# Optimization experiments

Measured on AMD Instinct MI355X. Metric: run time of the kernel, lower is better.

## Reference

```python
import jax, jax.numpy as jnp
import numpy as np

N = 50000      # nodes
E = 800000     # edges
IN = 128       # in_dim
OUT = 128      # out_dim
R = 4          # num_relations
H = 8          # heads
D = OUT // H   # per-head dim
NEG_SLOPE = 0.2


def setup_inputs() -> dict:
    key = jax.random.key(0)
    ks = jax.random.split(key, 12)
    s = 0.05
    return {
        "node_inp": jax.random.normal(ks[0], (N, IN), dtype=jnp.float32),
        "edge_index": jax.random.randint(ks[1], (2, E), 0, N),
        "edge_type": jax.random.randint(ks[2], (E,), 0, R),
        # per-relation GATConv params
        "W_rel": jax.random.normal(ks[3], (R, IN, OUT), dtype=jnp.float32) * s,
        "att_src_rel": jax.random.normal(ks[4], (R, H, D), dtype=jnp.float32) * s,
        "att_dst_rel": jax.random.normal(ks[5], (R, H, D), dtype=jnp.float32) * s,
        "bias_rel": jax.random.normal(ks[6], (R, OUT), dtype=jnp.float32) * s,
        # linear layers
        "W_self": jax.random.normal(ks[7], (IN, OUT), dtype=jnp.float32) * s,   # lin_self
        "W_cross": jax.random.normal(ks[8], (OUT, OUT), dtype=jnp.float32) * s,  # lin_cross
        # lang_conv GAT params (lin_l is Bypass, so no weight matrix)
        "att_src_lang": jax.random.normal(ks[9], (H, D), dtype=jnp.float32) * s,
        "att_dst_lang": jax.random.normal(ks[10], (H, D), dtype=jnp.float32) * s,
        "bias_lang": jax.random.normal(ks[11], (OUT,), dtype=jnp.float32) * s,
    }


def _hgnn_forward(node_inp, edge_index, edge_type, W_rel, att_src_rel,
                  att_dst_rel, bias_rel, W_self, W_cross,
                  att_src_lang, att_dst_lang, bias_lang):
    src, dst = edge_index[0], edge_index[1]

    def rel_gat(W, a_s, a_d, b, mask):
        # standard PyG GATConv (single x, add_self_loops=False), restricted to
        # edges with this relation type via mask
        x = (node_inp @ W).reshape(N, H, D)                     # [N,H,D]
        es = jnp.einsum('nhd,hd->nh', x, a_s)
        ed = jnp.einsum('nhd,hd->nh', x, a_d)
        logit = jax.nn.leaky_relu(es[src] + ed[dst], NEG_SLOPE)  # [E,H]
        logit = jnp.where(mask[:, None], logit, -1e30)
        mx = jax.ops.segment_max(logit, dst, num_segments=N)     # [N,H]
        mx = jnp.maximum(mx, -1e30)                              # avoid -inf
        p = jnp.exp(logit - mx[dst]) * mask[:, None]
        den = jax.ops.segment_sum(p, dst, num_segments=N)        # [N,H]
        alpha = p / jnp.where(den > 0, den, 1.0)[dst]            # [E,H]
        msg = alpha[..., None] * x[src]                          # [E,H,D]
        out = jax.ops.segment_sum(msg, dst, num_segments=N)      # [N,H,D]
        tmask = jax.ops.segment_sum(mask.astype(jnp.float32), dst,
                                    num_segments=N) > 0          # [N] target nodes
        return out.reshape(N, OUT) + b, tmask

    rel_masks = edge_type[None, :] == jnp.arange(R)[:, None]     # [R,E]
    rel_out, tmask = jax.vmap(rel_gat)(W_rel, att_src_rel, att_dst_rel,
                                       bias_rel, rel_masks)      # [R,N,OUT],[R,N]
    h = jax.nn.gelu(rel_out, approximate=False) @ W_cross        # [R,N,OUT]

    S = node_inp @ W_self                                        # [N,OUT] self entries
    # lang_conv: per node i, GAT attention over entries {self(i)} U
    # {rel outputs at i for relations where i is a target}. lin_l = Bypass,
    # and since x is a single tensor in PyG, x_dst = rel_inputs[i] = S[i].
    ent = jnp.concatenate([S[None], h], axis=0).reshape(R + 1, N, H, D)
    valid = jnp.concatenate([jnp.ones((1, N), bool), tmask], axis=0)  # [R+1,N]
    ls = jnp.einsum('knhd,hd->knh', ent, att_src_lang)
    ld = jnp.einsum('nhd,hd->nh', ent[0], att_dst_lang)
    logit = jax.nn.leaky_relu(ls + ld[None], NEG_SLOPE)          # [R+1,N,H]
    logit = jnp.where(valid[..., None], logit, -jnp.inf)
    alpha = jax.nn.softmax(logit, axis=0)                        # self always valid
    out = jnp.einsum('knh,knhd->nhd', alpha, ent).reshape(N, OUT)
    return out + bias_lang


def reference(node_inp, edge_index, edge_type, W_rel, att_src_rel, att_dst_rel,
              bias_rel, W_self, W_cross, att_src_lang, att_dst_lang, bias_lang):
    return _hgnn_forward(node_inp, edge_index, edge_type, W_rel, att_src_rel,
                         att_dst_rel, bias_rel, W_self, W_cross,
                         att_src_lang, att_dst_lang, bias_lang)
```

## Files before the change

### kernel.cpp

```cpp
#include <hip/hip_runtime.h>
#include <hip/hip_bf16.h>
#include <math.h>

#define NN 50000
#define NE 800000
#define NREL 4
#define NHEAD 8
#define NSEG (NREL * NN)
#define BCAP 26

typedef __hip_bfloat16 bf16;
typedef short short8 __attribute__((ext_vector_type(8)));
typedef float floatx4 __attribute__((ext_vector_type(4)));

#define LOG2E 1.4426950408889634f

__device__ __forceinline__ float b2f(bf16 v) { return __bfloat162float(v); }
__device__ __forceinline__ float us2f(unsigned short u) {
    return __uint_as_float(((unsigned)u) << 16);
}
__device__ __forceinline__ unsigned short f2us(float v) {
    bf16 b = __float2bfloat16(v);
    return *(unsigned short*)&b;
}

__device__ __forceinline__ float gelu_f(float v) {
    float z = v * 0.70710678118654752f;
    float az = fabsf(z);
    float t = __builtin_amdgcn_rcpf(__builtin_fmaf(0.3275911f, az, 1.f));
    float p = t * (0.254829592f +
              t * (-0.284496736f +
              t * (1.421413741f +
              t * (-1.453152027f +
              t * 1.061405429f))));
    float ex = __builtin_amdgcn_exp2f(az * az * -LOG2E);
    float er = copysignf(1.f - p * ex, z);
    return 0.5f * v * (1.f + er);
}

__global__ void fill_kernel(float* __restrict__ out, int n) {
    int t = blockIdx.x * blockDim.x + threadIdx.x;
    if (t < n) out[t] = 1000.0f;
}

__global__ void prep_kernel(const float* __restrict__ W_rel,
                            const float* __restrict__ W_self,
                            const float* __restrict__ W_cross,
                            const float* __restrict__ a_src,
                            const float* __restrict__ a_dst,
                            const float* __restrict__ node_inp,
                            bf16* __restrict__ Wt, bf16* __restrict__ Wct,
                            bf16* __restrict__ Ab,
                            int* __restrict__ counts) {
    int t = blockIdx.x * blockDim.x + threadIdx.x;
    if (t < NSEG) counts[t] = 0;
    if (t < 768 * 128) {
        int row = t >> 7, k = t & 127;
        float v;
        if (row < 512) {
            int r = row >> 7, c = row & 127;
            v = W_rel[(r * 128 + k) * 128 + c];
        } else if (row < 640) {
            v = W_self[k * 128 + (row - 512)];
        } else if (row < 704) {
            int q = row - 640;
            bool is_src = q < 32;
            int qq = is_src ? q : q - 32;
            int r = qq >> 3, h = qq & 7;
            const float* av = (is_src ? a_src : a_dst) + (r * 8 + h) * 16;
            const float* wr = W_rel + (size_t)(r * 128 + k) * 128 + h * 16;
            float s = 0.f;
            #pragma unroll
            for (int dd = 0; dd < 16; ++dd) s += wr[dd] * av[dd];
            v = s * LOG2E;
        } else {
            v = 0.f;
        }
        Wt[t] = __float2bfloat16(v);
    } else if (t < 768 * 128 + 128 * 128) {
        int u = t - 768 * 128;
        int n = u >> 7, k = u & 127;
        Wct[u] = __float2bfloat16(W_cross[k * 128 + n]);
    }
    if (t < NN * 16) {
        const float* ap = node_inp + (size_t)t * 8;
        float4 f0 = *(const float4*)ap;
        float4 f1 = *(const float4*)(ap + 4);
        short8 v = (short8){(short)f2us(f0.x), (short)f2us(f0.y),
                            (short)f2us(f0.z), (short)f2us(f0.w),
                            (short)f2us(f1.x), (short)f2us(f1.y),
                            (short)f2us(f1.z), (short)f2us(f1.w)};
        *(short8*)(Ab + (size_t)t * 8) = v;
    }
}

__global__ __launch_bounds__(256) void gemm_node(
    const bf16* __restrict__ Ab,
    const bf16* __restrict__ Bt,
    bf16* __restrict__ outb,
    float* __restrict__ outf,
    unsigned short* __restrict__ es_u,
    unsigned short* __restrict__ ed_u,
    const int* __restrict__ ei,
    const int* __restrict__ et,
    int* __restrict__ counts,
    unsigned short* __restrict__ bkt,
    int M)
{
    if (blockIdx.y == 0) {
        int idx = blockIdx.x * 256 + threadIdx.x;
        int stride = gridDim.x * 256;
        for (int e = idx; e < NE; e += stride) {
            int seg = et[e] * NN + ei[NE + e];
            int pos = atomicAdd(&counts[seg], 1);
            if (pos < BCAP) bkt[(unsigned)seg * BCAP + pos] = (unsigned short)ei[e];
        }
        return;
    }

    __shared__ __align__(16) char smem[25600];
    short (*As)[40] = (short (*)[40])smem;
    short (*Bs)[40] = (short (*)[40])(smem + 5120);

    const int tid  = threadIdx.x;
    const int wave = tid >> 6, lane = tid & 63;
    const int quad = lane >> 4, l16 = lane & 15;
    const int wr_ = wave & 1, wc = wave >> 1;
    const int row0 = blockIdx.x * 64;
    const int plane = blockIdx.y - 1;
    const int col0 = plane * 256;

    floatx4 acc[2][8];
    #pragma unroll
    for (int i = 0; i < 2; ++i)
        #pragma unroll
        for (int j = 0; j < 8; ++j) acc[i][j] = (floatx4){0.f, 0.f, 0.f, 0.f};

    for (int k0 = 0; k0 < 128; k0 += 32) {
        {
            int c = tid;
            int r = c >> 2, off = (c & 3) * 8;
            int gr = row0 + r;
            short8 v = {0, 0, 0, 0, 0, 0, 0, 0};
            if (gr < M)
                v = *(const short8*)(Ab + (((size_t)gr) << 7) + k0 + off);
            *(short8*)&As[r][off] = v;
        }
        #pragma unroll
        for (int i = 0; i < 4; ++i) {
            int c = i * 256 + tid;
            int r = c >> 2, off = (c & 3) * 8;
            short8 w = *(const short8*)(Bt + (((size_t)(col0 + r)) << 7) + k0 + off);
            *(short8*)&Bs[r][off] = w;
        }
        __syncthreads();

        short8 av[2], bv[8];
        #pragma unroll
        for (int mt = 0; mt < 2; ++mt)
            av[mt] = *(const short8*)&As[wr_ * 32 + mt * 16 + l16][quad * 8];
        #pragma unroll
        for (int nt = 0; nt < 8; ++nt)
            bv[nt] = *(const short8*)&Bs[wc * 128 + nt * 16 + l16][quad * 8];
        #pragma unroll
        for (int mt = 0; mt < 2; ++mt)
            #pragma unroll
            for (int nt = 0; nt < 8; ++nt)
                acc[mt][nt] = __builtin_amdgcn_mfma_f32_16x16x32_bf16(
                    av[mt], bv[nt], acc[mt][nt], 0, 0, 0);
        __syncthreads();
    }

    const bool eswave = (plane == 2 && wc == 1);
    if (eswave) {
        #pragma unroll
        for (int mt = 0; mt < 2; ++mt) {
            #pragma unroll
            for (int reg = 0; reg < 4; ++reg) {
                int gr = row0 + wr_ * 32 + mt * 16 + quad * 4 + reg;
                if (gr >= M) continue;
                #pragma unroll
                for (int nt = 0; nt < 4; ++nt) {
                    int q = nt * 16 + l16;
                    unsigned short v = f2us(acc[mt][nt][reg]);
                    if (q < 32)
                        es_u[(unsigned)((q >> 3) * NN + gr) * 8u + (unsigned)(q & 7)] = v;
                    else
                        ed_u[(unsigned)(((q - 32) >> 3) * NN + gr) * 8u + (unsigned)((q - 32) & 7)] = v;
                }
            }
        }
    }

    float* ct = (float*)(smem + wave * 4352);
    const int rr2 = lane >> 2;
    const int cc0 = (lane & 3) * 16;

    for (int mt = 0; mt < 2; ++mt) {
        #pragma unroll
        for (int half = 0; half < 2; ++half) {
            if (!eswave) {
                #pragma unroll
                for (int nt = 0; nt < 4; ++nt)
                    #pragma unroll
                    for (int reg = 0; reg < 4; ++reg)
                        ct[(quad * 4 + reg) * 68 + nt * 16 + l16] =
                            acc[mt][half * 4 + nt][reg];
            }
            __syncthreads();
            if (!eswave) {
                int gr2 = row0 + wr_ * 32 + mt * 16 + rr2;
                if (gr2 < M) {
                    float4 f0 = *(const float4*)&ct[rr2 * 68 + cc0];
                    float4 f1 = *(const float4*)&ct[rr2 * 68 + cc0 + 4];
                    float4 f2 = *(const float4*)&ct[rr2 * 68 + cc0 + 8];
                    float4 f3 = *(const float4*)&ct[rr2 * 68 + cc0 + 12];
                    int lc = half * 64 + cc0;
                    if (plane == 2) {
                        float* dst = outf + (((size_t)gr2) << 7) + lc;
                        ((float4*)dst)[0] = f0;
                        ((float4*)dst)[1] = f1;
                        ((float4*)dst)[2] = f2;
                        ((float4*)dst)[3] = f3;
                    } else {
                        int rel = plane * 2 + wc;
                        float tmp[16] = {f0.x, f0.y, f0.z, f0.w, f1.x, f1.y, f1.z, f1.w,
                                         f2.x, f2.y, f2.z, f2.w, f3.x, f3.y, f3.z, f3.w};
                        short8 o0, o1;
                        #pragma unroll
                        for (int j = 0; j < 8; ++j) o0[j] = (short)f2us(tmp[j]);
                        #pragma unroll
                        for (int j = 0; j < 8; ++j) o1[j] = (short)f2us(tmp[8 + j]);
                        bf16* dst = outb + ((size_t)(rel * NN + gr2) << 7) + lc;
                        *(short8*)dst = o0;
                        *(short8*)(dst + 8) = o1;
                    }
                }
            }
            __syncthreads();
        }
    }
}

__global__ __launch_bounds__(256) void agg_kernel(
    const unsigned short* __restrict__ bkt, const int* __restrict__ counts,
    const bf16* __restrict__ Xb, const unsigned short* __restrict__ es_u,
    const unsigned short* __restrict__ ed_u, const float* __restrict__ bias_rel,
    bf16* __restrict__ Gb4, unsigned char* __restrict__ flag)
{
    const int rel = blockIdx.y;
    const int n = blockIdx.x * 4 + (threadIdx.x >> 6);
    if (n >= NN) return;
    const int l = threadIdx.x & 63;
    const int h = l >> 3;
    const int f = l * 2;
    const unsigned seg = (unsigned)(rel * NN + n);
    int cnt = __builtin_amdgcn_readfirstlane(counts[seg]);
    cnt = cnt < BCAP ? cnt : BCAP;
    const unsigned short* bk = bkt + seg * (unsigned)BCAP;
    const float edv = us2f(ed_u[seg * 8u + (unsigned)h]);
    float a0 = 0.f, a1 = 0.f, den = 0.f;
    const unsigned short* Xr = (const unsigned short*)Xb + (unsigned)rel * (unsigned)(NN * 128);
    const unsigned short* esr = es_u + (unsigned)rel * (unsigned)(NN * 8);

    int e = 0;
    for (; e + 3 < cnt; e += 4) {
        int s0 = __builtin_amdgcn_readfirstlane((int)bk[e]);
        int s1 = __builtin_amdgcn_readfirstlane((int)bk[e + 1]);
        int s2 = __builtin_amdgcn_readfirstlane((int)bk[e + 2]);
        int s3 = __builtin_amdgcn_readfirstlane((int)bk[e + 3]);
        float e0 = us2f(esr[(unsigned)s0 * 8u + (unsigned)h]);
        float e1 = us2f(esr[(unsigned)s1 * 8u + (unsigned)h]);
        float e2 = us2f(esr[(unsigned)s2 * 8u + (unsigned)h]);
        float e3 = us2f(esr[(unsigned)s3 * 8u + (unsigned)h]);
        ushort2 u0 = *(const ushort2*)(Xr + (unsigned)s0 * 128u + (unsigned)f);
        ushort2 u1 = *(const ushort2*)(Xr + (unsigned)s1 * 128u + (unsigned)f);
        ushort2 u2 = *(const ushort2*)(Xr + (unsigned)s2 * 128u + (unsigned)f);
        ushort2 u3 = *(const ushort2*)(Xr + (unsigned)s3 * 128u + (unsigned)f);
        float aa0 = e0 + edv, aa1 = e1 + edv, aa2 = e2 + edv, aa3 = e3 + edv;
        float w0 = __builtin_amdgcn_exp2f(fmaxf(aa0, 0.2f * aa0));
        float w1 = __builtin_amdgcn_exp2f(fmaxf(aa1, 0.2f * aa1));
        float w2 = __builtin_amdgcn_exp2f(fmaxf(aa2, 0.2f * aa2));
        float w3 = __builtin_amdgcn_exp2f(fmaxf(aa3, 0.2f * aa3));
        a0 += w0 * us2f(u0.x) + w1 * us2f(u1.x) + w2 * us2f(u2.x) + w3 * us2f(u3.x);
        a1 += w0 * us2f(u0.y) + w1 * us2f(u1.y) + w2 * us2f(u2.y) + w3 * us2f(u3.y);
        den += (w0 + w1) + (w2 + w3);
    }
    for (; e < cnt; ++e) {
        int s0 = __builtin_amdgcn_readfirstlane((int)bk[e]);
        float e0 = us2f(esr[(unsigned)s0 * 8u + (unsigned)h]);
        ushort2 u0 = *(const ushort2*)(Xr + (unsigned)s0 * 128u + (unsigned)f);
        float aa0 = e0 + edv;
        float w0 = __builtin_amdgcn_exp2f(fmaxf(aa0, 0.2f * aa0));
        a0 += w0 * us2f(u0.x);
        a1 += w0 * us2f(u0.y);
        den += w0;
    }

    float inv = den > 0.f ? __builtin_amdgcn_rcpf(den) : 0.f;
    float2 bv = *(const float2*)(bias_rel + (unsigned)rel * 128u + (unsigned)f);
    float v0 = gelu_f(__builtin_fmaf(a0, inv, bv.x));
    float v1 = gelu_f(__builtin_fmaf(a1, inv, bv.y));
    ushort2 o;
    o.x = f2us(v0);
    o.y = f2us(v1);
    *(ushort2*)((unsigned short*)Gb4 + ((unsigned)n * 4u + (unsigned)rel) * 128u + (unsigned)f) = o;
    if (l == 0) flag[(unsigned)n * 4u + (unsigned)rel] = (unsigned char)(cnt > 0);
}

__global__ __launch_bounds__(256) void gemm_lang(
    const bf16* __restrict__ A,
    const bf16* __restrict__ Bt,
    const unsigned char* __restrict__ flag,
    const float* __restrict__ asl_g,
    const float* __restrict__ adl_g,
    const float* __restrict__ bias_lang,
    float* __restrict__ out)
{
    __shared__ __align__(16) char smem[15360];
    short (*As)[40] = (short (*)[40])smem;
    short (*Bs)[40] = (short (*)[40])(smem + 5120);

    const int M = NN * NREL;
    const int tid  = threadIdx.x;
    const int wave = tid >> 6, lane = tid & 63;
    const int quad = lane >> 4, l16 = lane & 15;
    const int wr_ = wave & 1, wc = wave >> 1;
    const int row0 = blockIdx.x * 64;

    floatx4 acc[2][4];
    #pragma unroll
    for (int i = 0; i < 2; ++i)
        #pragma unroll
        for (int j = 0; j < 4; ++j) acc[i][j] = (floatx4){0.f, 0.f, 0.f, 0.f};

    for (int k0 = 0; k0 < 128; k0 += 32) {
        {
            int c = tid;
            int r = c >> 2, off = (c & 3) * 8;
            int gr = row0 + r;
            short8 v = {0, 0, 0, 0, 0, 0, 0, 0};
            if (gr < M)
                v = *(const short8*)(A + (((size_t)gr) << 7) + k0 + off);
            *(short8*)&As[r][off] = v;
        }
        #pragma unroll
        for (int i = 0; i < 2; ++i) {
            int c = tid * 2 + i;
            int r = c >> 2, off = (c & 3) * 8;
            short8 w = *(const short8*)(Bt + (((size_t)r) << 7) + k0 + off);
            *(short8*)&Bs[r][off] = w;
        }
        __syncthreads();

        short8 av[2], bv[4];
        #pragma unroll
        for (int mt = 0; mt < 2; ++mt)
            av[mt] = *(const short8*)&As[wr_ * 32 + mt * 16 + l16][quad * 8];
        #pragma unroll
        for (int nt = 0; nt < 4; ++nt)
            bv[nt] = *(const short8*)&Bs[wc * 64 + nt * 16 + l16][quad * 8];
        #pragma unroll
        for (int mt = 0; mt < 2; ++mt)
            #pragma unroll
            for (int nt = 0; nt < 4; ++nt)
                acc[mt][nt] = __builtin_amdgcn_mfma_f32_16x16x32_bf16(
                    av[mt], bv[nt], acc[mt][nt], 0, 0, 0);
        __syncthreads();
    }

    const int nb0 = blockIdx.x * 16 + wr_ * 8;
    #pragma unroll
    for (int nt = 0; nt < 4; ++nt) {
        int col = wc * 64 + nt * 16 + l16;
        float asl = asl_g[col];
        float adl = adl_g[col];
        float bl  = bias_lang[col];
        #pragma unroll
        for (int mt = 0; mt < 2; ++mt) {
            int node = nb0 + mt * 4 + quad;
            bool ok = node < NN;
            float Sv = ok ? out[(unsigned)node * 128u + (unsigned)col] : 0.f;
            float h0 = acc[mt][nt][0], h1 = acc[mt][nt][1];
            float h2 = acc[mt][nt][2], h3 = acc[mt][nt][3];
            float t0 = h0 * asl, t1 = h1 * asl, t2 = h2 * asl, t3 = h3 * asl;
            float ts = Sv * asl, td = Sv * adl;
            #pragma unroll
            for (int off = 1; off < 16; off <<= 1) {
                t0 += __shfl_xor(t0, off);
                t1 += __shfl_xor(t1, off);
                t2 += __shfl_xor(t2, off);
                t3 += __shfl_xor(t3, off);
                ts += __shfl_xor(ts, off);
                td += __shfl_xor(td, off);
            }
            unsigned fl = ok ? *(const unsigned*)(flag + (unsigned)node * 4u) : 0u;
            float aS = ts + td, a0 = t0 + td, a1 = t1 + td, a2 = t2 + td, a3 = t3 + td;
            float lS = fmaxf(aS, 0.2f * aS);
            float l0 = fmaxf(a0, 0.2f * a0);
            float l1 = fmaxf(a1, 0.2f * a1);
            float l2 = fmaxf(a2, 0.2f * a2);
            float l3 = fmaxf(a3, 0.2f * a3);
            bool v0 = (fl & 0x000000FFu) != 0, v1 = (fl & 0x0000FF00u) != 0;
            bool v2 = (fl & 0x00FF0000u) != 0, v3 = (fl & 0xFF000000u) != 0;
            float m = lS;
            if (v0) m = fmaxf(m, l0);
            if (v1) m = fmaxf(m, l1);
            if (v2) m = fmaxf(m, l2);
            if (v3) m = fmaxf(m, l3);
            float eS = __expf(lS - m);
            float e0 = v0 ? __expf(l0 - m) : 0.f;
            float e1 = v1 ? __expf(l1 - m) : 0.f;
            float e2 = v2 ? __expf(l2 - m) : 0.f;
            float e3 = v3 ? __expf(l3 - m) : 0.f;
            float sum = eS + e0 + e1 + e2 + e3;
            float o = eS * Sv + e0 * h0 + e1 * h1 + e2 * h2 + e3 * h3;
            o = o / sum + bl;
            if (ok) out[(unsigned)node * 128u + (unsigned)col] = o;
        }
    }
}

extern "C" void kernel_launch(void* const* d_in, const int* in_sizes, int n_in,
                              void* d_out, int out_size, void* d_ws, size_t ws_size,
                              hipStream_t stream) {
    const float* node_inp     = (const float*)d_in[0];
    const int*   edge_index   = (const int*)d_in[1];
    const int*   edge_type    = (const int*)d_in[2];
    const float* W_rel        = (const float*)d_in[3];
    const float* att_src_rel  = (const float*)d_in[4];
    const float* att_dst_rel  = (const float*)d_in[5];
    const float* bias_rel     = (const float*)d_in[6];
    const float* W_self       = (const float*)d_in[7];
    const float* W_cross      = (const float*)d_in[8];
    const float* att_src_lang = (const float*)d_in[9];
    const float* att_dst_lang = (const float*)d_in[10];
    const float* bias_lang    = (const float*)d_in[11];
    (void)in_sizes; (void)n_in;

    const size_t SZ_XB   = (size_t)NREL * NN * 128 * 2;
    const size_t SZ_ES   = (size_t)NREL * NN * 8 * 2;
    const size_t SZ_GB4  = (size_t)NREL * NN * 128 * 2;
    const size_t SZ_WT   = 768 * 128 * 2;
    const size_t SZ_WCT  = 128 * 128 * 2;
    const size_t SZ_BKT  = (size_t)NSEG * BCAP * 2;
    const size_t SZ_CNT  = (size_t)NSEG * 4;
    const size_t SZ_FLG  = (size_t)NN * 4;
    const size_t TOTAL = SZ_XB + 2 * SZ_ES + SZ_GB4 + SZ_WT + SZ_WCT +
                         SZ_BKT + SZ_CNT + SZ_FLG;

    if (ws_size < TOTAL) {
        fill_kernel<<<(out_size + 255) / 256, 256, 0, stream>>>((float*)d_out, out_size);
        return;
    }

    char* ws = (char*)d_ws;
    size_t o = 0;
    bf16*  Xb      = (bf16*)(ws + o);  o += SZ_XB;
    unsigned short* es_u = (unsigned short*)(ws + o); o += SZ_ES;
    unsigned short* ed_u = (unsigned short*)(ws + o); o += SZ_ES;
    bf16*  Gb4     = (bf16*)(ws + o);  o += SZ_GB4;
    bf16*  Wt      = (bf16*)(ws + o);  o += SZ_WT;
    bf16*  Wct     = (bf16*)(ws + o);  o += SZ_WCT;
    unsigned short* bkt = (unsigned short*)(ws + o); o += SZ_BKT;
    int*   counts  = (int*)(ws + o);   o += SZ_CNT;
    unsigned char* flag = (unsigned char*)(ws + o);
    float* S       = (float*)d_out;
    bf16*  Ab      = Gb4;

    prep_kernel<<<(NN * 16 + 255) / 256, 256, 0, stream>>>(
        W_rel, W_self, W_cross, att_src_rel, att_dst_rel, node_inp,
        Wt, Wct, Ab, counts);

    dim3 g1((NN + 63) / 64, 4);
    gemm_node<<<g1, 256, 0, stream>>>(Ab, Wt, Xb, S, es_u, ed_u,
                                      edge_index, edge_type, counts, bkt, NN);

    dim3 ga((NN + 3) / 4, NREL);
    agg_kernel<<<ga, 256, 0, stream>>>(bkt, counts, Xb, es_u, ed_u, bias_rel, Gb4, flag);

    dim3 g2((NREL * NN + 63) / 64, 1);
    gemm_lang<<<g2, 256, 0, stream>>>(Gb4, Wct, flag, att_src_lang, att_dst_lang,
                                      bias_lang, (float*)d_out);
}
```

Before: 312.5 us.

## Move edge bucketing scatter from GEMM kernel into prep kernel

The edge bucketing (atomic count plus source write per relation/destination segment) moves out of a dedicated blockIdx.y==0 plane of the node GEMM launch and into the prep kernel. Each thread now handles one edge, with the atomic issued early so its latency overlaps the weight and input conversion work. Zeroing the counts is done by a hipMemsetAsync, because the atomics now run in the same kernel that used to clear them. The GEMM grid shrinks to three planes, at the cost of a larger prep grid and an extra memset launch.

Result: faster. 289.8 us (-7.3%).

```diff
diff --git a/kernel.cpp b/kernel.cpp
--- a/kernel.cpp
+++ b/kernel.cpp
@@ -43,17 +43,30 @@
     if (t < n) out[t] = 1000.0f;
 }
 
-__global__ void prep_kernel(const float* __restrict__ W_rel,
-                            const float* __restrict__ W_self,
-                            const float* __restrict__ W_cross,
-                            const float* __restrict__ a_src,
-                            const float* __restrict__ a_dst,
-                            const float* __restrict__ node_inp,
-                            bf16* __restrict__ Wt, bf16* __restrict__ Wct,
-                            bf16* __restrict__ Ab,
-                            int* __restrict__ counts) {
+__global__ __launch_bounds__(256) void prep_scatter(
+    const float* __restrict__ W_rel,
+    const float* __restrict__ W_self,
+    const float* __restrict__ W_cross,
+    const float* __restrict__ a_src,
+    const float* __restrict__ a_dst,
+    const float* __restrict__ node_inp,
+    const int* __restrict__ ei,
+    const int* __restrict__ et,
+    bf16* __restrict__ Wt, bf16* __restrict__ Wct,
+    bf16* __restrict__ Ab,
+    int* __restrict__ counts,
+    unsigned short* __restrict__ bkt) {
     int t = blockIdx.x * blockDim.x + threadIdx.x;
-    if (t < NSEG) counts[t] = 0;
+
+    int src = 0, pos = BCAP;
+    unsigned seg = 0;
+    if (t < NE) {
+        src = ei[t];
+        int dst = ei[NE + t];
+        seg = (unsigned)(et[t] * NN + dst);
+        pos = atomicAdd(&counts[seg], 1);
+    }
+
     if (t < 768 * 128) {
         int row = t >> 7, k = t & 127;
         float v;
@@ -82,6 +95,7 @@
         int n = u >> 7, k = u & 127;
         Wct[u] = __float2bfloat16(W_cross[k * 128 + n]);
     }
+
     if (t < NN * 16) {
         const float* ap = node_inp + (size_t)t * 8;
         float4 f0 = *(const float4*)ap;
@@ -92,6 +106,9 @@
                             (short)f2us(f1.z), (short)f2us(f1.w)};
         *(short8*)(Ab + (size_t)t * 8) = v;
     }
+
+    if (t < NE && pos < BCAP)
+        bkt[seg * (unsigned)BCAP + (unsigned)pos] = (unsigned short)src;
 }
 
 __global__ __launch_bounds__(256) void gemm_node(
@@ -101,23 +118,8 @@
     float* __restrict__ outf,
     unsigned short* __restrict__ es_u,
     unsigned short* __restrict__ ed_u,
-    const int* __restrict__ ei,
-    const int* __restrict__ et,
-    int* __restrict__ counts,
-    unsigned short* __restrict__ bkt,
     int M)
 {
-    if (blockIdx.y == 0) {
-        int idx = blockIdx.x * 256 + threadIdx.x;
-        int stride = gridDim.x * 256;
-        for (int e = idx; e < NE; e += stride) {
-            int seg = et[e] * NN + ei[NE + e];
-            int pos = atomicAdd(&counts[seg], 1);
-            if (pos < BCAP) bkt[(unsigned)seg * BCAP + pos] = (unsigned short)ei[e];
-        }
-        return;
-    }
-
     __shared__ __align__(16) char smem[25600];
     short (*As)[40] = (short (*)[40])smem;
     short (*Bs)[40] = (short (*)[40])(smem + 5120);
@@ -127,7 +129,7 @@
     const int quad = lane >> 4, l16 = lane & 15;
     const int wr_ = wave & 1, wc = wave >> 1;
     const int row0 = blockIdx.x * 64;
-    const int plane = blockIdx.y - 1;
+    const int plane = blockIdx.y;
     const int col0 = plane * 256;
 
     floatx4 acc[2][8];
@@ -468,13 +470,14 @@
     float* S       = (float*)d_out;
     bf16*  Ab      = Gb4;
 
-    prep_kernel<<<(NN * 16 + 255) / 256, 256, 0, stream>>>(
+    hipMemsetAsync(counts, 0, SZ_CNT, stream);
+
+    prep_scatter<<<(NE + 255) / 256, 256, 0, stream>>>(
         W_rel, W_self, W_cross, att_src_rel, att_dst_rel, node_inp,
-        Wt, Wct, Ab, counts);
-
-    dim3 g1((NN + 63) / 64, 4);
-    gemm_node<<<g1, 256, 0, stream>>>(Ab, Wt, Xb, S, es_u, ed_u,
-                                      edge_index, edge_type, counts, bkt, NN);
+        edge_index, edge_type, Wt, Wct, Ab, counts, bkt);
+
+    dim3 g1((NN + 63) / 64, 3);
+    gemm_node<<<g1, 256, 0, stream>>>(Ab, Wt, Xb, S, es_u, ed_u, NN);
 
     dim3 ga((NN + 3) / 4, NREL);
     agg_kernel<<<ga, 256, 0, stream>>>(bkt, counts, Xb, es_u, ed_u, bias_rel, Gb4, flag);
```
